# Kernel optimization log

Hardware: AMD Instinct MI355X
Metric: run time of the kernel (lower is better)

The kernel has to match this reference:

```python
import jax, jax.numpy as jnp
import numpy as np

N = 524288
L = 16            # encoding levels
F = 2             # features per level
LOG2_T = 19
T = 2 ** LOG2_T   # hash table size per level
BASE_RES = 16
FINEST = BASE_RES * 2 ** (L - 1)
WIDTH = 64
DENSITY_OUT = 16

# corner offsets of a voxel, i (x) outer, k (z) inner -- matches BOX_OFFSETS
OFFSETS = jnp.array([[i, j, k] for i in (0, 1) for j in (0, 1) for k in (0, 1)], dtype=jnp.int32)  # [8,3]
# primes wrapped to int32 exactly as jax x32 canonicalization does in the original
PRIMES = jnp.asarray(np.array([1, 2654435761, 805459861], dtype=np.int64).astype(np.int32))
_b = np.exp((np.log(FINEST) - np.log(BASE_RES)) / (L - 1))
RESOLUTIONS = jnp.asarray(np.floor(BASE_RES * _b ** np.arange(L)).astype(np.float32))  # [L]


def sh_encode(d):
    """Spherical harmonic encoding, degree 4 -> [N,25], faithful to source coeffs."""
    x, y, z = d[..., 0:1], d[..., 1:2], d[..., 2:3]
    x2, y2, z2 = x * x, y * y, z * z
    xy, xz, yz = x * y, x * z, y * z
    x4, y4 = x2 * x2, y2 * y2
    out = [jnp.full_like(x, 0.5 * np.sqrt(1.0 / np.pi))]
    c1 = 0.5 * np.sqrt(3.0 / np.pi)
    out += [-c1 * y, c1 * z, -c1 * x]
    sub = 0.25 * np.sqrt(5.0 / np.pi)
    v1 = 0.25 * np.sqrt(15.0 / np.pi)
    v2 = 0.5 * np.sqrt(15.0 / np.pi)
    v3 = 0.75 * np.sqrt(5.0 / np.pi)
    out += [v2 * xy, -v2 * yz, v3 * z2 - sub, -v2 * xz, v1 * x2 - v1 * y2]
    w1 = 0.25 * np.sqrt(105.0 / np.pi)
    w2 = 0.5 * np.sqrt(105.0 / np.pi)
    w3 = 0.25 * np.sqrt(35.0 / (2.0 * np.pi))
    w4 = 0.5 * np.sqrt(7.0 / (6.0 * np.pi))
    out += [-w3 * y * (3.0 * x2 - y2), w2 * xy * z, w4 * y * (1.5 - 7.5 * z2),
            1.24392110863372 * z * (1.5 * z2 - 0.5) - 0.497568443453487 * z,
            w4 * x * (1.5 - 7.5 * z2), w1 * z * (x2 - y2), -w3 * x * (x2 - 3.0 * y2)]
    out += [2.5033429417967 * xy * (x2 - y2),
            -1.77013076977993 * yz * (3.0 * x2 - y2),
            0.126156626101008 * xy * (52.5 * z2 - 7.5),
            0.267618617422916 * y * (2.33333333333333 * z * (1.5 - 7.5 * z2) + 4.0 * z),
            1.48099765681286 * z * (1.66666666666667 * z * (1.5 * z2 - 0.5) - 0.666666666666667 * z) - 0.952069922236839 * z2 + 0.317356640745613,
            0.267618617422916 * x * (2.33333333333333 * z * (1.5 - 7.5 * z2) + 4.0 * z),
            0.063078313050504 * (x2 - y2) * (52.5 * z2 - 7.5),
            -1.77013076977993 * xz * (x2 - 3.0 * y2),
            -3.75501441269506 * x2 * y2 + 0.625835735449176 * x4 + 0.625835735449176 * y4]
    return jnp.concatenate(out, axis=-1)  # [N,25]


def hash_grid_encode(x, tables):
    """x: [N,3] in unit cube; tables: [L,T,F] -> [N, L*F]."""
    def level(table, res):
        grid = 1.0 / res                              # box is [0,1]^3
        bl = jnp.floor(x / grid).astype(jnp.int32)    # bottom-left voxel index [N,3]
        w = (x - bl.astype(x.dtype) * grid) / grid    # trilinear weights [N,3]
        idx = bl[:, None, :] + OFFSETS[None]          # [N,8,3]
        h = ((idx[..., 0] * PRIMES[0]) ^ (idx[..., 1] * PRIMES[1]) ^ (idx[..., 2] * PRIMES[2])) % T
        emb = table[h]                                # [N,8,F] gather
        cw = jnp.where(OFFSETS[None].astype(bool), w[:, None, :], 1.0 - w[:, None, :]).prod(-1)  # [N,8]
        return jnp.einsum('ncf,nc->nf', emb, cw)
    feats = jax.vmap(level)(tables, RESOLUTIONS)      # [L,N,F]
    return jnp.transpose(feats, (1, 0, 2)).reshape(x.shape[0], L * F)


def setup_inputs() -> dict:
    key = jax.random.key(0)
    ks = jax.random.split(key, 8)
    position = jax.random.uniform(ks[0], (N, 3), jnp.float32)
    direction = jax.random.normal(ks[1], (N, 3), jnp.float32)
    hash_tables = jax.random.uniform(ks[2], (L, T, F), jnp.float32, -1e-4, 1e-4)
    def dense(k, fan_in, fan_out):
        return (jax.random.normal(k, (fan_in, fan_out), jnp.float32) / np.sqrt(fan_in),
                jnp.zeros((fan_out,), jnp.float32))
    W_d1, b_d1 = dense(ks[3], L * F, WIDTH)
    W_d2, b_d2 = dense(ks[4], WIDTH, DENSITY_OUT)
    W_c1, b_c1 = dense(ks[5], DENSITY_OUT + 25, WIDTH)
    W_c2, b_c2 = dense(ks[6], WIDTH, WIDTH)
    W_c3, b_c3 = dense(ks[7], WIDTH, 3)
    return dict(position=position, direction=direction, hash_tables=hash_tables,
                W_d1=W_d1, b_d1=b_d1, W_d2=W_d2, b_d2=b_d2,
                W_c1=W_c1, b_c1=b_c1, W_c2=W_c2, b_c2=b_c2, W_c3=W_c3, b_c3=b_c3)


def reference(position, direction, hash_tables, W_d1, b_d1, W_d2, b_d2,
              W_c1, b_c1, W_c2, b_c2, W_c3, b_c3):
    enc_pos = hash_grid_encode(position, hash_tables)     # [N,32]
    enc_dir = sh_encode(direction)                        # [N,25]
    y = jax.nn.relu(enc_pos @ W_d1 + b_d1)                # density MLP (1 hidden layer)
    density_out = y @ W_d2 + b_d2                         # [N,16]
    sigma = jax.nn.relu(density_out[:, -1:])              # [N,1]
    h = jnp.concatenate([density_out, enc_dir], axis=-1)  # [N,41]
    h = jax.nn.relu(h @ W_c1 + b_c1)
    h = jax.nn.relu(h @ W_c2 + b_c2)
    rgb = jax.nn.sigmoid(h @ W_c3 + b_c3)                 # [N,3]
    return (rgb, sigma)
```

## Files before the change

kernel.cpp:

```cpp
#include <hip/hip_runtime.h>
#include <math.h>

#define LEVELS 16
#define TBL 524288
#define TMASK (TBL - 1)

typedef short bf16x8 __attribute__((ext_vector_type(8)));
typedef float f32x4  __attribute__((ext_vector_type(4)));
typedef float fvec4  __attribute__((ext_vector_type(4)));
typedef unsigned int uvec4 __attribute__((ext_vector_type(4)));

static __device__ __forceinline__ unsigned short f2bf(float x) {
    unsigned u = __float_as_uint(x);
    u += 0x7fffu + ((u >> 16) & 1u);
    return (unsigned short)(u >> 16);
}
static __device__ __forceinline__ float b2f(unsigned short h) {
    return __uint_as_float(((unsigned)h) << 16);
}

#define SH_BLOCK(sh, dx, dy, dz)                                                          \
    const float x2 = dx * dx, y2 = dy * dy, z2 = dz * dz;                                 \
    const float xy = dx * dy, xz = dx * dz, yz = dy * dz;                                 \
    const float x4 = x2 * x2, y4 = y2 * y2;                                               \
    const float c0  = (float)(0.5 * sqrt(1.0 / M_PI));                                    \
    const float c1  = (float)(0.5 * sqrt(3.0 / M_PI));                                    \
    const float sub = (float)(0.25 * sqrt(5.0 / M_PI));                                   \
    const float v1  = (float)(0.25 * sqrt(15.0 / M_PI));                                  \
    const float v2  = (float)(0.5 * sqrt(15.0 / M_PI));                                   \
    const float v3  = (float)(0.75 * sqrt(5.0 / M_PI));                                   \
    const float w1c = (float)(0.25 * sqrt(105.0 / M_PI));                                 \
    const float w2c = (float)(0.5 * sqrt(105.0 / M_PI));                                  \
    const float w3c = (float)(0.25 * sqrt(35.0 / (2.0 * M_PI)));                          \
    const float w4c = (float)(0.5 * sqrt(7.0 / (6.0 * M_PI)));                            \
    sh[0] = c0;                                                                           \
    sh[1] = -c1 * dy;                                                                     \
    sh[2] =  c1 * dz;                                                                     \
    sh[3] = -c1 * dx;                                                                     \
    sh[4] =  v2 * xy;                                                                     \
    sh[5] = -v2 * yz;                                                                     \
    sh[6] =  v3 * z2 - sub;                                                               \
    sh[7] = -v2 * xz;                                                                     \
    sh[8] =  v1 * x2 - v1 * y2;                                                           \
    sh[9]  = -w3c * dy * (3.0f * x2 - y2);                                                \
    sh[10] =  w2c * xy * dz;                                                              \
    sh[11] =  w4c * dy * (1.5f - 7.5f * z2);                                              \
    sh[12] =  1.24392110863372f * dz * (1.5f * z2 - 0.5f) - 0.497568443453487f * dz;      \
    sh[13] =  w4c * dx * (1.5f - 7.5f * z2);                                              \
    sh[14] =  w1c * dz * (x2 - y2);                                                       \
    sh[15] = -w3c * dx * (x2 - 3.0f * y2);                                                \
    sh[16] =  2.5033429417967f * xy * (x2 - y2);                                          \
    sh[17] = -1.77013076977993f * yz * (3.0f * x2 - y2);                                  \
    sh[18] =  0.126156626101008f * xy * (52.5f * z2 - 7.5f);                              \
    sh[19] =  0.267618617422916f * dy * (2.33333333333333f * dz * (1.5f - 7.5f * z2) + 4.0f * dz); \
    sh[20] =  1.48099765681286f * dz * (1.66666666666667f * dz * (1.5f * z2 - 0.5f) - 0.666666666666667f * dz) \
              - 0.952069922236839f * z2 + 0.317356640745613f;                             \
    sh[21] =  0.267618617422916f * dx * (2.33333333333333f * dz * (1.5f - 7.5f * z2) + 4.0f * dz); \
    sh[22] =  0.063078313050504f * (x2 - y2) * (52.5f * z2 - 7.5f);                       \
    sh[23] = -1.77013076977993f * xz * (x2 - 3.0f * y2);                                  \
    sh[24] = -3.75501441269506f * x2 * y2 + 0.625835735449176f * x4 + 0.625835735449176f * y4;

__global__ __launch_bounds__(256)
void cvt_tables(const float* __restrict__ tables,
                unsigned int* __restrict__ tb16, int total)
{
    const int i = (blockIdx.x * 256 + threadIdx.x) * 4;
    if (i >= total) return;
    const fvec4 a = __builtin_nontemporal_load((const fvec4*)(tables + 2 * (size_t)i));
    const fvec4 b = __builtin_nontemporal_load((const fvec4*)(tables + 2 * (size_t)i) + 1);
    uvec4 o;
    o.x = ((unsigned)f2bf(a.y) << 16) | f2bf(a.x);
    o.y = ((unsigned)f2bf(a.w) << 16) | f2bf(a.z);
    o.z = ((unsigned)f2bf(b.y) << 16) | f2bf(b.x);
    o.w = ((unsigned)f2bf(b.w) << 16) | f2bf(b.z);
    __builtin_nontemporal_store(o, (uvec4*)&tb16[i]);
}

__global__ __launch_bounds__(256)
void ngp_encode_lvl(const float* __restrict__ pos,
                    const unsigned int* __restrict__ tb16,
                    unsigned int* __restrict__ wsp, int n)
{
    const int b = blockIdx.x;
    const int p = b & 7;
    const int h = b >> 14;
    const int l = 2 * p + h;
    const int c = (b & 16383) >> 3;
    const int idx = c * 256 + threadIdx.x;
    if (idx >= n || l >= LEVELS) return;

    const float px = pos[3 * idx + 0];
    const float py = pos[3 * idx + 1];
    const float pz = pos[3 * idx + 2];

    const float resf = (float)(16 << l);
    const float tx = px * resf, ty = py * resf, tz = pz * resf;
    const float fx = floorf(tx), fy = floorf(ty), fz = floorf(tz);
    const float wx = tx - fx, wy = ty - fy, wz = tz - fz;
    const unsigned ix = (unsigned)(int)fx;
    const unsigned iy = (unsigned)(int)fy;
    const unsigned iz = (unsigned)(int)fz;
    const unsigned hy0 = iy * 2654435761u, hy1 = hy0 + 2654435761u;
    const unsigned hz0 = iz * 805459861u,  hz1 = hz0 + 805459861u;
    const unsigned ix1 = ix + 1u;

    const unsigned int* tb = tb16 + (size_t)l * TBL;
    const unsigned hA = hy0 ^ hz0;
    const unsigned hB = hy0 ^ hz1;
    const unsigned hC = hy1 ^ hz0;
    const unsigned hD = hy1 ^ hz1;

    unsigned eA0, eA1, eB0, eB1, eC0, eC1, eD0, eD1;
    if ((ix & 1u) == 0u) {
        const uint2 pA = *(const uint2*)&tb[((ix ^ hA) & TMASK) & ~1u];
        const uint2 pB = *(const uint2*)&tb[((ix ^ hB) & TMASK) & ~1u];
        const uint2 pC = *(const uint2*)&tb[((ix ^ hC) & TMASK) & ~1u];
        const uint2 pD = *(const uint2*)&tb[((ix ^ hD) & TMASK) & ~1u];
        const unsigned sA = hA & 1u, sB = hB & 1u, sC = hC & 1u, sD = hD & 1u;
        eA0 = sA ? pA.y : pA.x;  eA1 = sA ? pA.x : pA.y;
        eB0 = sB ? pB.y : pB.x;  eB1 = sB ? pB.x : pB.y;
        eC0 = sC ? pC.y : pC.x;  eC1 = sC ? pC.x : pC.y;
        eD0 = sD ? pD.y : pD.x;  eD1 = sD ? pD.x : pD.y;
    } else {
        eA0 = tb[(ix  ^ hA) & TMASK];  eA1 = tb[(ix1 ^ hA) & TMASK];
        eB0 = tb[(ix  ^ hB) & TMASK];  eB1 = tb[(ix1 ^ hB) & TMASK];
        eC0 = tb[(ix  ^ hC) & TMASK];  eC1 = tb[(ix1 ^ hC) & TMASK];
        eD0 = tb[(ix  ^ hD) & TMASK];  eD1 = tb[(ix1 ^ hD) & TMASK];
    }

#define UNPX(e) __uint_as_float((e) << 16)
#define UNPY(e) __uint_as_float((e) & 0xffff0000u)

    const float ux = 1.f - wx, uy = 1.f - wy, uz = 1.f - wz;
    const float c000 = ux * uy * uz, c001 = ux * uy * wz;
    const float c010 = ux * wy * uz, c011 = ux * wy * wz;
    const float c100 = wx * uy * uz, c101 = wx * uy * wz;
    const float c110 = wx * wy * uz, c111 = wx * wy * wz;

    float f0 = UNPX(eA0) * c000, f1 = UNPY(eA0) * c000;
    f0 = fmaf(UNPX(eB0), c001, f0); f1 = fmaf(UNPY(eB0), c001, f1);
    f0 = fmaf(UNPX(eC0), c010, f0); f1 = fmaf(UNPY(eC0), c010, f1);
    f0 = fmaf(UNPX(eD0), c011, f0); f1 = fmaf(UNPY(eD0), c011, f1);
    f0 = fmaf(UNPX(eA1), c100, f0); f1 = fmaf(UNPY(eA1), c100, f1);
    f0 = fmaf(UNPX(eB1), c101, f0); f1 = fmaf(UNPY(eB1), c101, f1);
    f0 = fmaf(UNPX(eC1), c110, f0); f1 = fmaf(UNPY(eC1), c110, f1);
    f0 = fmaf(UNPX(eD1), c111, f0); f1 = fmaf(UNPY(eD1), c111, f1);

    const unsigned int h0 = f2bf(f0);
    const unsigned int h1 = f2bf(f1);
    __builtin_nontemporal_store((h1 << 16) | h0, &wsp[(size_t)l * n + idx]);
}

#define MT   512
#define GROUPS 8
#define SW1  32
#define SW   72
#define SA   68
#define OW1  0
#define OW2  2048
#define OC1H 3200
#define OC1L 7808
#define OC2H 12416
#define OC2L 17024
#define OC3H 21632
#define OC3L 21920
#define WTOT 22208

__global__ __launch_bounds__(512, 4)
void ngp_mlp_mfma4(const unsigned int* __restrict__ wsp,
                   const float* __restrict__ dirp,
                   const float* __restrict__ Wd1, const float* __restrict__ bd1,
                   const float* __restrict__ Wd2, const float* __restrict__ bd2,
                   const float* __restrict__ Wc1, const float* __restrict__ bc1,
                   const float* __restrict__ Wc2, const float* __restrict__ bc2,
                   const float* __restrict__ Wc3, const float* __restrict__ bc3,
                   float* __restrict__ out, int n)
{
    __shared__ short wsm[WTOT];
    __shared__ float act[8 * 16 * SA];
    const int tid = threadIdx.x;

    for (int t = tid; t < WTOT; t += MT) wsm[t] = 0;
    __syncthreads();

    for (int g = tid; g < 32 * 64; g += MT) {
        const int k = g >> 6, nn = g & 63;
        wsm[OW1 + nn * SW1 + k] = f2bf(Wd1[g]);
    }
    for (int g = tid; g < 64 * 16; g += MT) {
        const int k = g >> 4, nn = g & 15;
        wsm[OW2 + nn * SW + k] = f2bf(Wd2[g]);
    }
    for (int g = tid; g < 41 * 64; g += MT) {
        const int k = g >> 6, nn = g & 63;
        const float w = Wc1[g];
        const unsigned short hh = f2bf(w);
        wsm[OC1H + nn * SW + k] = hh;
        wsm[OC1L + nn * SW + k] = f2bf(w - b2f(hh));
    }
    for (int g = tid; g < 64 * 64; g += MT) {
        const int k = g >> 6, nn = g & 63;
        const float w = Wc2[g];
        const unsigned short hh = f2bf(w);
        wsm[OC2H + nn * SW + k] = hh;
        wsm[OC2L + nn * SW + k] = f2bf(w - b2f(hh));
    }
    for (int g = tid; g < 64 * 3; g += MT) {
        const int k = g / 3, nn = g - 3 * k;
        const float w = Wc3[g];
        const unsigned short hh = f2bf(w);
        wsm[OC3H + nn * SW + k] = hh;
        wsm[OC3L + nn * SW + k] = f2bf(w - b2f(hh));
    }
    __syncthreads();

    const int wid = tid >> 6;
    const int lane = tid & 63;
    const int ln = lane & 15;
    const int qd = lane >> 4;
    float* A = act + wid * (16 * SA);

    float bd1v[4], bc1v[4], bc2v[4];
#pragma unroll
    for (int t = 0; t < 4; ++t) {
        bd1v[t] = bd1[t * 16 + ln];
        bc1v[t] = bc1[t * 16 + ln];
        bc2v[t] = bc2[t * 16 + ln];
    }
    const float bd2v = bd2[ln];
    const float bc3v = (ln < 3) ? bc3[ln] : 0.f;

#define LOAD_SPLIT(ah, al, k0)                                   \
    {                                                            \
        _Pragma("unroll")                                        \
        for (int j = 0; j < 8; ++j) {                            \
            const float v = A[ln * SA + (k0) + j];               \
            const unsigned short hb = f2bf(v);                   \
            ah[j] = (short)hb;                                   \
            al[j] = (short)f2bf(v - b2f(hb));                    \
        }                                                        \
    }

#define SPLIT_TILE(acc, ah0, ah1, al0, al1, OH, OL, row)                                          \
    {                                                                                             \
        const bf16x8 bh0 = *(const bf16x8*)&wsm[(OH) + (row) * SW + qd * 8];                      \
        const bf16x8 bh1 = *(const bf16x8*)&wsm[(OH) + (row) * SW + 32 + qd * 8];                 \
        acc = __builtin_amdgcn_mfma_f32_16x16x32_bf16(ah0, bh0, acc, 0, 0, 0);                    \
        acc = __builtin_amdgcn_mfma_f32_16x16x32_bf16(ah1, bh1, acc, 0, 0, 0);                    \
        acc = __builtin_amdgcn_mfma_f32_16x16x32_bf16(al0, bh0, acc, 0, 0, 0);                    \
        acc = __builtin_amdgcn_mfma_f32_16x16x32_bf16(al1, bh1, acc, 0, 0, 0);                    \
        const bf16x8 bl0 = *(const bf16x8*)&wsm[(OL) + (row) * SW + qd * 8];                      \
        const bf16x8 bl1 = *(const bf16x8*)&wsm[(OL) + (row) * SW + 32 + qd * 8];                 \
        acc = __builtin_amdgcn_mfma_f32_16x16x32_bf16(ah0, bl0, acc, 0, 0, 0);                    \
        acc = __builtin_amdgcn_mfma_f32_16x16x32_bf16(ah1, bl1, acc, 0, 0, 0);                    \
    }

    const int pt0 = blockIdx.x * (GROUPS * 128) + wid * 16 + ln;
    unsigned int xu0, xu1, xu2, xu3;
    float dq0, dq1, dq2;
    xu0 = wsp[(size_t)(qd * 4 + 0) * n + pt0];
    xu1 = wsp[(size_t)(qd * 4 + 1) * n + pt0];
    xu2 = wsp[(size_t)(qd * 4 + 2) * n + pt0];
    xu3 = wsp[(size_t)(qd * 4 + 3) * n + pt0];
    dq0 = dirp[3 * pt0 + 0];
    dq1 = dirp[3 * pt0 + 1];
    dq2 = dirp[3 * pt0 + 2];

#pragma unroll 1
    for (int grp = 0; grp < GROUPS; ++grp) {
        const int pt_base = blockIdx.x * (GROUPS * 128) + grp * 128 + wid * 16;
        const int pt = pt_base + ln;

        bf16x8 ax;
        ax[0] = (short)(xu0 & 0xffffu); ax[1] = (short)(xu0 >> 16);
        ax[2] = (short)(xu1 & 0xffffu); ax[3] = (short)(xu1 >> 16);
        ax[4] = (short)(xu2 & 0xffffu); ax[5] = (short)(xu2 >> 16);
        ax[6] = (short)(xu3 & 0xffffu); ax[7] = (short)(xu3 >> 16);
        const float ddx = dq0, ddy = dq1, ddz = dq2;

        if (grp + 1 < GROUPS) {
            const int ptn = pt + 128;
            xu0 = wsp[(size_t)(qd * 4 + 0) * n + ptn];
            xu1 = wsp[(size_t)(qd * 4 + 1) * n + ptn];
            xu2 = wsp[(size_t)(qd * 4 + 2) * n + ptn];
            xu3 = wsp[(size_t)(qd * 4 + 3) * n + ptn];
            dq0 = dirp[3 * ptn + 0];
            dq1 = dirp[3 * ptn + 1];
            dq2 = dirp[3 * ptn + 2];
        }

#pragma unroll
        for (int t = 0; t < 4; ++t) {
            const bf16x8 b = *(const bf16x8*)&wsm[OW1 + (t * 16 + ln) * SW1 + qd * 8];
            const float bv = bd1v[t];
            f32x4 acc = {bv, bv, bv, bv};
            acc = __builtin_amdgcn_mfma_f32_16x16x32_bf16(ax, b, acc, 0, 0, 0);
#pragma unroll
            for (int r = 0; r < 4; ++r)
                A[(qd * 4 + r) * SA + t * 16 + ln] = fmaxf(acc[r], 0.f);
        }

        {
            bf16x8 a0, a1;
#pragma unroll
            for (int j = 0; j < 8; ++j) a0[j] = (short)f2bf(A[ln * SA + qd * 8 + j]);
#pragma unroll
            for (int j = 0; j < 8; ++j) a1[j] = (short)f2bf(A[ln * SA + 32 + qd * 8 + j]);
            const bf16x8 b0 = *(const bf16x8*)&wsm[OW2 + ln * SW + qd * 8];
            const bf16x8 b1 = *(const bf16x8*)&wsm[OW2 + ln * SW + 32 + qd * 8];
            const float bv = bd2v;
            f32x4 acc = {bv, bv, bv, bv};
            acc = __builtin_amdgcn_mfma_f32_16x16x32_bf16(a0, b0, acc, 0, 0, 0);
            acc = __builtin_amdgcn_mfma_f32_16x16x32_bf16(a1, b1, acc, 0, 0, 0);
            if (ln == 15) {
#pragma unroll
                for (int r = 0; r < 4; ++r)
                    out[3 * n + pt_base + qd * 4 + r] = fmaxf(acc[r], 0.f);
            }
#pragma unroll
            for (int r = 0; r < 4; ++r)
                A[(qd * 4 + r) * SA + ln] = acc[r];
        }

        {
            const float dxv = ddx, dyv = ddy, dzv = ddz;
            const float x2 = dxv * dxv, y2 = dyv * dyv, z2 = dzv * dzv;
            const float xy = dxv * dyv, xz = dxv * dzv, yz = dyv * dzv;
            const float x4 = x2 * x2, y4 = y2 * y2;
            const float c0  = (float)(0.5 * sqrt(1.0 / M_PI));
            const float c1  = (float)(0.5 * sqrt(3.0 / M_PI));
            const float sub = (float)(0.25 * sqrt(5.0 / M_PI));
            const float v1  = (float)(0.25 * sqrt(15.0 / M_PI));
            const float v2  = (float)(0.5 * sqrt(15.0 / M_PI));
            const float v3  = (float)(0.75 * sqrt(5.0 / M_PI));
            const float w1c = (float)(0.25 * sqrt(105.0 / M_PI));
            const float w2c = (float)(0.5 * sqrt(105.0 / M_PI));
            const float w3c = (float)(0.25 * sqrt(35.0 / (2.0 * M_PI)));
            const float w4c = (float)(0.5 * sqrt(7.0 / (6.0 * M_PI)));
            float* Ash = &A[ln * SA + 16];
#define SH_PUT(i, expr) { if (((i) & 3) == qd) Ash[i] = (expr); }
            SH_PUT(0,  c0)
            SH_PUT(1,  -c1 * dyv)
            SH_PUT(2,   c1 * dzv)
            SH_PUT(3,  -c1 * dxv)
            SH_PUT(4,   v2 * xy)
            SH_PUT(5,  -v2 * yz)
            SH_PUT(6,   v3 * z2 - sub)
            SH_PUT(7,  -v2 * xz)
            SH_PUT(8,   v1 * x2 - v1 * y2)
            SH_PUT(9,  -w3c * dyv * (3.0f * x2 - y2))
            SH_PUT(10,  w2c * xy * dzv)
            SH_PUT(11,  w4c * dyv * (1.5f - 7.5f * z2))
            SH_PUT(12,  1.24392110863372f * dzv * (1.5f * z2 - 0.5f) - 0.497568443453487f * dzv)
            SH_PUT(13,  w4c * dxv * (1.5f - 7.5f * z2))
            SH_PUT(14,  w1c * dzv * (x2 - y2))
            SH_PUT(15, -w3c * dxv * (x2 - 3.0f * y2))
            SH_PUT(16,  2.5033429417967f * xy * (x2 - y2))
            SH_PUT(17, -1.77013076977993f * yz * (3.0f * x2 - y2))
            SH_PUT(18,  0.126156626101008f * xy * (52.5f * z2 - 7.5f))
            SH_PUT(19,  0.267618617422916f * dyv * (2.33333333333333f * dzv * (1.5f - 7.5f * z2) + 4.0f * dzv))
            SH_PUT(20,  1.48099765681286f * dzv * (1.66666666666667f * dzv * (1.5f * z2 - 0.5f) - 0.666666666666667f * dzv)
                        - 0.952069922236839f * z2 + 0.317356640745613f)
            SH_PUT(21,  0.267618617422916f * dxv * (2.33333333333333f * dzv * (1.5f - 7.5f * z2) + 4.0f * dzv))
            SH_PUT(22,  0.063078313050504f * (x2 - y2) * (52.5f * z2 - 7.5f))
            SH_PUT(23, -1.77013076977993f * xz * (x2 - 3.0f * y2))
            SH_PUT(24, -3.75501441269506f * x2 * y2 + 0.625835735449176f * x4 + 0.625835735449176f * y4)
#undef SH_PUT
        }

        {
            bf16x8 ah0, ah1, al0, al1;
            LOAD_SPLIT(ah0, al0, qd * 8)
            LOAD_SPLIT(ah1, al1, 32 + qd * 8)
#pragma unroll
            for (int t = 0; t < 4; ++t) {
                const float bv = bc1v[t];
                f32x4 acc = {bv, bv, bv, bv};
                SPLIT_TILE(acc, ah0, ah1, al0, al1, OC1H, OC1L, t * 16 + ln)
#pragma unroll
                for (int r = 0; r < 4; ++r)
                    A[(qd * 4 + r) * SA + t * 16 + ln] = fmaxf(acc[r], 0.f);
                __builtin_amdgcn_sched_barrier(0);
            }
        }

        {
            bf16x8 ah0, ah1, al0, al1;
            LOAD_SPLIT(ah0, al0, qd * 8)
            LOAD_SPLIT(ah1, al1, 32 + qd * 8)
#pragma unroll
            for (int t = 0; t < 4; ++t) {
                const float bv = bc2v[t];
                f32x4 acc = {bv, bv, bv, bv};
                SPLIT_TILE(acc, ah0, ah1, al0, al1, OC2H, OC2L, t * 16 + ln)
#pragma unroll
                for (int r = 0; r < 4; ++r)
                    A[(qd * 4 + r) * SA + t * 16 + ln] = fmaxf(acc[r], 0.f);
                __builtin_amdgcn_sched_barrier(0);
            }
        }

        {
            bf16x8 ah0, ah1, al0, al1;
            LOAD_SPLIT(ah0, al0, qd * 8)
            LOAD_SPLIT(ah1, al1, 32 + qd * 8)
            const float bv = bc3v;
            f32x4 acc = {bv, bv, bv, bv};
            SPLIT_TILE(acc, ah0, ah1, al0, al1, OC3H, OC3L, (ln & 3))
            if (ln < 3) {
#pragma unroll
                for (int r = 0; r < 4; ++r)
                    out[3 * (pt_base + qd * 4 + r) + ln] = 1.f / (1.f + expf(-acc[r]));
            }
        }
    }
}

__global__ __launch_bounds__(256)
void nerf_fused(const float* __restrict__ pos,
                const float* __restrict__ dirp,
                const float* __restrict__ tables,
                const float* __restrict__ Wd1, const float* __restrict__ bd1,
                const float* __restrict__ Wd2, const float* __restrict__ bd2,
                const float* __restrict__ Wc1, const float* __restrict__ bc1,
                const float* __restrict__ Wc2, const float* __restrict__ bc2,
                const float* __restrict__ Wc3, const float* __restrict__ bc3,
                float* __restrict__ out, int n)
{
    const int idx = blockIdx.x * blockDim.x + threadIdx.x;
    if (idx >= n) return;
    const float px = pos[3 * idx + 0], py = pos[3 * idx + 1], pz = pos[3 * idx + 2];
    float y[64];
#pragma unroll
    for (int j = 0; j < 64; ++j) y[j] = bd1[j];
#pragma unroll
    for (int l = 0; l < LEVELS; ++l) {
        const float resf = (float)(16 << l);
        const float tx = px * resf, ty = py * resf, tz = pz * resf;
        const float fx = floorf(tx), fy = floorf(ty), fz = floorf(tz);
        const float wx = tx - fx, wy = ty - fy, wz = tz - fz;
        const unsigned ix = (unsigned)(int)fx, iy = (unsigned)(int)fy, iz = (unsigned)(int)fz;
        const unsigned hy0 = iy * 2654435761u, hy1 = hy0 + 2654435761u;
        const unsigned hz0 = iz * 805459861u,  hz1 = hz0 + 805459861u;
        const unsigned ix1 = ix + 1u;
        const float2* tb = (const float2*)tables + (size_t)l * TBL;
        const float2 e000 = tb[(ix  ^ hy0 ^ hz0) & TMASK];
        const float2 e001 = tb[(ix  ^ hy0 ^ hz1) & TMASK];
        const float2 e010 = tb[(ix  ^ hy1 ^ hz0) & TMASK];
        const float2 e011 = tb[(ix  ^ hy1 ^ hz1) & TMASK];
        const float2 e100 = tb[(ix1 ^ hy0 ^ hz0) & TMASK];
        const float2 e101 = tb[(ix1 ^ hy0 ^ hz1) & TMASK];
        const float2 e110 = tb[(ix1 ^ hy1 ^ hz0) & TMASK];
        const float2 e111 = tb[(ix1 ^ hy1 ^ hz1) & TMASK];
        const float ux = 1.f - wx, uy = 1.f - wy, uz = 1.f - wz;
        const float c000 = ux*uy*uz, c001 = ux*uy*wz, c010 = ux*wy*uz, c011 = ux*wy*wz;
        const float c100 = wx*uy*uz, c101 = wx*uy*wz, c110 = wx*wy*uz, c111 = wx*wy*wz;
        float f0 = e000.x*c000, f1 = e000.y*c000;
        f0 = fmaf(e001.x,c001,f0); f1 = fmaf(e001.y,c001,f1);
        f0 = fmaf(e010.x,c010,f0); f1 = fmaf(e010.y,c010,f1);
        f0 = fmaf(e011.x,c011,f0); f1 = fmaf(e011.y,c011,f1);
        f0 = fmaf(e100.x,c100,f0); f1 = fmaf(e100.y,c100,f1);
        f0 = fmaf(e101.x,c101,f0); f1 = fmaf(e101.y,c101,f1);
        f0 = fmaf(e110.x,c110,f0); f1 = fmaf(e110.y,c110,f1);
        f0 = fmaf(e111.x,c111,f0); f1 = fmaf(e111.y,c111,f1);
        const float* w0 = Wd1 + (size_t)(2 * l) * 64;
#pragma unroll
        for (int j = 0; j < 64; ++j)
            y[j] = fmaf(f0, w0[j], fmaf(f1, w0[64 + j], y[j]));
    }
    float d[16];
#pragma unroll
    for (int k = 0; k < 16; ++k) d[k] = bd2[k];
#pragma unroll
    for (int j = 0; j < 64; ++j) {
        const float a = fmaxf(y[j], 0.f);
#pragma unroll
        for (int k = 0; k < 16; ++k) d[k] = fmaf(a, Wd2[j * 16 + k], d[k]);
    }
    out[3 * n + idx] = fmaxf(d[15], 0.f);
    const float dx = dirp[3*idx], dy = dirp[3*idx+1], dz = dirp[3*idx+2];
    float sh[25];
    SH_BLOCK(sh, dx, dy, dz)
    float h1[64];
#pragma unroll
    for (int j = 0; j < 64; ++j) h1[j] = bc1[j];
#pragma unroll
    for (int i = 0; i < 16; ++i) {
#pragma unroll
        for (int j = 0; j < 64; ++j) h1[j] = fmaf(d[i], Wc1[i * 64 + j], h1[j]);
    }
#pragma unroll
    for (int s = 0; s < 25; ++s) {
#pragma unroll
        for (int j = 0; j < 64; ++j) h1[j] = fmaf(sh[s], Wc1[(16 + s) * 64 + j], h1[j]);
    }
    float h2[64];
#pragma unroll
    for (int j = 0; j < 64; ++j) h2[j] = bc2[j];
#pragma unroll
    for (int i = 0; i < 64; ++i) {
        const float a = fmaxf(h1[i], 0.f);
#pragma unroll
        for (int j = 0; j < 64; ++j) h2[j] = fmaf(a, Wc2[i * 64 + j], h2[j]);
    }
    float r0 = bc3[0], r1 = bc3[1], r2 = bc3[2];
#pragma unroll
    for (int j = 0; j < 64; ++j) {
        const float a = fmaxf(h2[j], 0.f);
        r0 = fmaf(a, Wc3[j * 3 + 0], r0);
        r1 = fmaf(a, Wc3[j * 3 + 1], r1);
        r2 = fmaf(a, Wc3[j * 3 + 2], r2);
    }
    out[3 * idx + 0] = 1.f / (1.f + expf(-r0));
    out[3 * idx + 1] = 1.f / (1.f + expf(-r1));
    out[3 * idx + 2] = 1.f / (1.f + expf(-r2));
}

extern "C" void kernel_launch(void* const* d_in, const int* in_sizes, int n_in,
                              void* d_out, int out_size, void* d_ws, size_t ws_size,
                              hipStream_t stream) {
    const float* pos    = (const float*)d_in[0];
    const float* dir    = (const float*)d_in[1];
    const float* tables = (const float*)d_in[2];
    const float* Wd1 = (const float*)d_in[3];
    const float* bd1 = (const float*)d_in[4];
    const float* Wd2 = (const float*)d_in[5];
    const float* bd2 = (const float*)d_in[6];
    const float* Wc1 = (const float*)d_in[7];
    const float* bc1 = (const float*)d_in[8];
    const float* Wc2 = (const float*)d_in[9];
    const float* bc2 = (const float*)d_in[10];
    const float* Wc3 = (const float*)d_in[11];
    const float* bc3 = (const float*)d_in[12];

    const int n = in_sizes[0] / 3;
    const int blocks = (n + 255) / 256;

    if (ws_size >= (size_t)n * 128 && n == 524288) {
        unsigned int* wsp  = (unsigned int*)d_ws;
        unsigned int* tb16 = (unsigned int*)((char*)d_ws + (size_t)n * 64);
        const int total = LEVELS * TBL;
        cvt_tables<<<total / 1024, 256, 0, stream>>>(tables, tb16, total);
        ngp_encode_lvl<<<16 * blocks, 256, 0, stream>>>(pos, tb16, wsp, n);
        ngp_mlp_mfma4<<<n / (128 * GROUPS), MT, 0, stream>>>((const unsigned int*)wsp, dir,
                                                             Wd1, bd1, Wd2, bd2,
                                                             Wc1, bc1, Wc2, bc2, Wc3, bc3,
                                                             (float*)d_out, n);
    } else {
        nerf_fused<<<blocks, 256, 0, stream>>>(pos, dir, tables,
                                               Wd1, bd1, Wd2, bd2,
                                               Wc1, bc1, Wc2, bc2, Wc3, bc3,
                                               (float*)d_out, n);
    }
}
```

Before: 355.3 us.

## Fuse hash-grid encoding into MLP kernel via shared-memory feature staging

```diff
diff --git a/kernel.cpp b/kernel.cpp
--- a/kernel.cpp
+++ b/kernel.cpp
@@ -76,83 +76,7 @@
     __builtin_nontemporal_store(o, (uvec4*)&tb16[i]);
 }
 
-__global__ __launch_bounds__(256)
-void ngp_encode_lvl(const float* __restrict__ pos,
-                    const unsigned int* __restrict__ tb16,
-                    unsigned int* __restrict__ wsp, int n)
-{
-    const int b = blockIdx.x;
-    const int p = b & 7;
-    const int h = b >> 14;
-    const int l = 2 * p + h;
-    const int c = (b & 16383) >> 3;
-    const int idx = c * 256 + threadIdx.x;
-    if (idx >= n || l >= LEVELS) return;
-
-    const float px = pos[3 * idx + 0];
-    const float py = pos[3 * idx + 1];
-    const float pz = pos[3 * idx + 2];
-
-    const float resf = (float)(16 << l);
-    const float tx = px * resf, ty = py * resf, tz = pz * resf;
-    const float fx = floorf(tx), fy = floorf(ty), fz = floorf(tz);
-    const float wx = tx - fx, wy = ty - fy, wz = tz - fz;
-    const unsigned ix = (unsigned)(int)fx;
-    const unsigned iy = (unsigned)(int)fy;
-    const unsigned iz = (unsigned)(int)fz;
-    const unsigned hy0 = iy * 2654435761u, hy1 = hy0 + 2654435761u;
-    const unsigned hz0 = iz * 805459861u,  hz1 = hz0 + 805459861u;
-    const unsigned ix1 = ix + 1u;
-
-    const unsigned int* tb = tb16 + (size_t)l * TBL;
-    const unsigned hA = hy0 ^ hz0;
-    const unsigned hB = hy0 ^ hz1;
-    const unsigned hC = hy1 ^ hz0;
-    const unsigned hD = hy1 ^ hz1;
-
-    unsigned eA0, eA1, eB0, eB1, eC0, eC1, eD0, eD1;
-    if ((ix & 1u) == 0u) {
-        const uint2 pA = *(const uint2*)&tb[((ix ^ hA) & TMASK) & ~1u];
-        const uint2 pB = *(const uint2*)&tb[((ix ^ hB) & TMASK) & ~1u];
-        const uint2 pC = *(const uint2*)&tb[((ix ^ hC) & TMASK) & ~1u];
-        const uint2 pD = *(const uint2*)&tb[((ix ^ hD) & TMASK) & ~1u];
-        const unsigned sA = hA & 1u, sB = hB & 1u, sC = hC & 1u, sD = hD & 1u;
-        eA0 = sA ? pA.y : pA.x;  eA1 = sA ? pA.x : pA.y;
-        eB0 = sB ? pB.y : pB.x;  eB1 = sB ? pB.x : pB.y;
-        eC0 = sC ? pC.y : pC.x;  eC1 = sC ? pC.x : pC.y;
-        eD0 = sD ? pD.y : pD.x;  eD1 = sD ? pD.x : pD.y;
-    } else {
-        eA0 = tb[(ix  ^ hA) & TMASK];  eA1 = tb[(ix1 ^ hA) & TMASK];
-        eB0 = tb[(ix  ^ hB) & TMASK];  eB1 = tb[(ix1 ^ hB) & TMASK];
-        eC0 = tb[(ix  ^ hC) & TMASK];  eC1 = tb[(ix1 ^ hC) & TMASK];
-        eD0 = tb[(ix  ^ hD) & TMASK];  eD1 = tb[(ix1 ^ hD) & TMASK];
-    }
-
-#define UNPX(e) __uint_as_float((e) << 16)
-#define UNPY(e) __uint_as_float((e) & 0xffff0000u)
-
-    const float ux = 1.f - wx, uy = 1.f - wy, uz = 1.f - wz;
-    const float c000 = ux * uy * uz, c001 = ux * uy * wz;
-    const float c010 = ux * wy * uz, c011 = ux * wy * wz;
-    const float c100 = wx * uy * uz, c101 = wx * uy * wz;
-    const float c110 = wx * wy * uz, c111 = wx * wy * wz;
-
-    float f0 = UNPX(eA0) * c000, f1 = UNPY(eA0) * c000;
-    f0 = fmaf(UNPX(eB0), c001, f0); f1 = fmaf(UNPY(eB0), c001, f1);
-    f0 = fmaf(UNPX(eC0), c010, f0); f1 = fmaf(UNPY(eC0), c010, f1);
-    f0 = fmaf(UNPX(eD0), c011, f0); f1 = fmaf(UNPY(eD0), c011, f1);
-    f0 = fmaf(UNPX(eA1), c100, f0); f1 = fmaf(UNPY(eA1), c100, f1);
-    f0 = fmaf(UNPX(eB1), c101, f0); f1 = fmaf(UNPY(eB1), c101, f1);
-    f0 = fmaf(UNPX(eC1), c110, f0); f1 = fmaf(UNPY(eC1), c110, f1);
-    f0 = fmaf(UNPX(eD1), c111, f0); f1 = fmaf(UNPY(eD1), c111, f1);
-
-    const unsigned int h0 = f2bf(f0);
-    const unsigned int h1 = f2bf(f1);
-    __builtin_nontemporal_store((h1 << 16) | h0, &wsp[(size_t)l * n + idx]);
-}
-
-#define MT   512
-#define GROUPS 8
+#define GROUPS_F 4
 #define SW1  32
 #define SW   72
 #define SA   68
@@ -166,51 +90,116 @@
 #define OC3L 21920
 #define WTOT 22208
 
-__global__ __launch_bounds__(512, 4)
-void ngp_mlp_mfma4(const unsigned int* __restrict__ wsp,
-                   const float* __restrict__ dirp,
-                   const float* __restrict__ Wd1, const float* __restrict__ bd1,
-                   const float* __restrict__ Wd2, const float* __restrict__ bd2,
-                   const float* __restrict__ Wc1, const float* __restrict__ bc1,
-                   const float* __restrict__ Wc2, const float* __restrict__ bc2,
-                   const float* __restrict__ Wc3, const float* __restrict__ bc3,
-                   float* __restrict__ out, int n)
+__global__ __launch_bounds__(256, 2)
+void ngp_fused(const float* __restrict__ pos,
+               const unsigned int* __restrict__ tb16,
+               const float* __restrict__ dirp,
+               const float* __restrict__ Wd1, const float* __restrict__ bd1,
+               const float* __restrict__ Wd2, const float* __restrict__ bd2,
+               const float* __restrict__ Wc1, const float* __restrict__ bc1,
+               const float* __restrict__ Wc2, const float* __restrict__ bc2,
+               const float* __restrict__ Wc3, const float* __restrict__ bc3,
+               float* __restrict__ out, int n)
 {
     __shared__ short wsm[WTOT];
-    __shared__ float act[8 * 16 * SA];
+    __shared__ unsigned int xf[256 * 16];
+    __shared__ float act[4 * 16 * SA];
     const int tid = threadIdx.x;
 
-    for (int t = tid; t < WTOT; t += MT) wsm[t] = 0;
+    for (int t = tid; t < WTOT; t += 256) wsm[t] = 0;
     __syncthreads();
-
-    for (int g = tid; g < 32 * 64; g += MT) {
+    for (int g = tid; g < 32 * 64; g += 256) {
         const int k = g >> 6, nn = g & 63;
         wsm[OW1 + nn * SW1 + k] = f2bf(Wd1[g]);
     }
-    for (int g = tid; g < 64 * 16; g += MT) {
+    for (int g = tid; g < 64 * 16; g += 256) {
         const int k = g >> 4, nn = g & 15;
         wsm[OW2 + nn * SW + k] = f2bf(Wd2[g]);
     }
-    for (int g = tid; g < 41 * 64; g += MT) {
+    for (int g = tid; g < 41 * 64; g += 256) {
         const int k = g >> 6, nn = g & 63;
         const float w = Wc1[g];
         const unsigned short hh = f2bf(w);
         wsm[OC1H + nn * SW + k] = hh;
         wsm[OC1L + nn * SW + k] = f2bf(w - b2f(hh));
     }
-    for (int g = tid; g < 64 * 64; g += MT) {
+    for (int g = tid; g < 64 * 64; g += 256) {
         const int k = g >> 6, nn = g & 63;
         const float w = Wc2[g];
         const unsigned short hh = f2bf(w);
         wsm[OC2H + nn * SW + k] = hh;
         wsm[OC2L + nn * SW + k] = f2bf(w - b2f(hh));
     }
-    for (int g = tid; g < 64 * 3; g += MT) {
+    for (int g = tid; g < 64 * 3; g += 256) {
         const int k = g / 3, nn = g - 3 * k;
         const float w = Wc3[g];
         const unsigned short hh = f2bf(w);
         wsm[OC3H + nn * SW + k] = hh;
         wsm[OC3L + nn * SW + k] = f2bf(w - b2f(hh));
+    }
+
+    {
+        const int ptg = blockIdx.x * 256 + tid;
+        const float px = pos[3 * ptg + 0];
+        const float py = pos[3 * ptg + 1];
+        const float pz = pos[3 * ptg + 2];
+#pragma unroll 2
+        for (int l = 0; l < LEVELS; ++l) {
+            const float resf = (float)(16 << l);
+            const float tx = px * resf, ty = py * resf, tz = pz * resf;
+            const float fx = floorf(tx), fy = floorf(ty), fz = floorf(tz);
+            const float wx = tx - fx, wy = ty - fy, wz = tz - fz;
+            const unsigned ix = (unsigned)(int)fx;
+            const unsigned iy = (unsigned)(int)fy;
+            const unsigned iz = (unsigned)(int)fz;
+            const unsigned hy0 = iy * 2654435761u, hy1 = hy0 + 2654435761u;
+            const unsigned hz0 = iz * 805459861u,  hz1 = hz0 + 805459861u;
+            const unsigned ix1 = ix + 1u;
+
+            const unsigned int* tb = tb16 + (size_t)l * TBL;
+            const unsigned hA = hy0 ^ hz0;
+            const unsigned hB = hy0 ^ hz1;
+            const unsigned hC = hy1 ^ hz0;
+            const unsigned hD = hy1 ^ hz1;
+
+            unsigned eA0, eA1, eB0, eB1, eC0, eC1, eD0, eD1;
+            if ((ix & 1u) == 0u) {
+                const uint2 pA = *(const uint2*)&tb[((ix ^ hA) & TMASK) & ~1u];
+                const uint2 pB = *(const uint2*)&tb[((ix ^ hB) & TMASK) & ~1u];
+                const uint2 pC = *(const uint2*)&tb[((ix ^ hC) & TMASK) & ~1u];
+                const uint2 pD = *(const uint2*)&tb[((ix ^ hD) & TMASK) & ~1u];
+                const unsigned sA = hA & 1u, sB = hB & 1u, sC = hC & 1u, sD = hD & 1u;
+                eA0 = sA ? pA.y : pA.x;  eA1 = sA ? pA.x : pA.y;
+                eB0 = sB ? pB.y : pB.x;  eB1 = sB ? pB.x : pB.y;
+                eC0 = sC ? pC.y : pC.x;  eC1 = sC ? pC.x : pC.y;
+                eD0 = sD ? pD.y : pD.x;  eD1 = sD ? pD.x : pD.y;
+            } else {
+                eA0 = tb[(ix  ^ hA) & TMASK];  eA1 = tb[(ix1 ^ hA) & TMASK];
+                eB0 = tb[(ix  ^ hB) & TMASK];  eB1 = tb[(ix1 ^ hB) & TMASK];
+                eC0 = tb[(ix  ^ hC) & TMASK];  eC1 = tb[(ix1 ^ hC) & TMASK];
+                eD0 = tb[(ix  ^ hD) & TMASK];  eD1 = tb[(ix1 ^ hD) & TMASK];
+            }
+
+#define UNPX(e) __uint_as_float((e) << 16)
+#define UNPY(e) __uint_as_float((e) & 0xffff0000u)
+
+            const float ux = 1.f - wx, uy = 1.f - wy, uz = 1.f - wz;
+            const float c000 = ux * uy * uz, c001 = ux * uy * wz;
+            const float c010 = ux * wy * uz, c011 = ux * wy * wz;
+            const float c100 = wx * uy * uz, c101 = wx * uy * wz;
+            const float c110 = wx * wy * uz, c111 = wx * wy * wz;
+
+            float f0 = UNPX(eA0) * c000, f1 = UNPY(eA0) * c000;
+            f0 = fmaf(UNPX(eB0), c001, f0); f1 = fmaf(UNPY(eB0), c001, f1);
+            f0 = fmaf(UNPX(eC0), c010, f0); f1 = fmaf(UNPY(eC0), c010, f1);
+            f0 = fmaf(UNPX(eD0), c011, f0); f1 = fmaf(UNPY(eD0), c011, f1);
+            f0 = fmaf(UNPX(eA1), c100, f0); f1 = fmaf(UNPY(eA1), c100, f1);
+            f0 = fmaf(UNPX(eB1), c101, f0); f1 = fmaf(UNPY(eB1), c101, f1);
+            f0 = fmaf(UNPX(eC1), c110, f0); f1 = fmaf(UNPY(eC1), c110, f1);
+            f0 = fmaf(UNPX(eD1), c111, f0); f1 = fmaf(UNPY(eD1), c111, f1);
+
+            xf[tid * 16 + l] = ((unsigned)f2bf(f1) << 16) | f2bf(f0);
+        }
     }
     __syncthreads();
 
@@ -255,35 +244,29 @@
         acc = __builtin_amdgcn_mfma_f32_16x16x32_bf16(ah1, bl1, acc, 0, 0, 0);                    \
     }
 
-    const int pt0 = blockIdx.x * (GROUPS * 128) + wid * 16 + ln;
-    unsigned int xu0, xu1, xu2, xu3;
-    float dq0, dq1, dq2;
-    xu0 = wsp[(size_t)(qd * 4 + 0) * n + pt0];
-    xu1 = wsp[(size_t)(qd * 4 + 1) * n + pt0];
-    xu2 = wsp[(size_t)(qd * 4 + 2) * n + pt0];
-    xu3 = wsp[(size_t)(qd * 4 + 3) * n + pt0];
-    dq0 = dirp[3 * pt0 + 0];
-    dq1 = dirp[3 * pt0 + 1];
-    dq2 = dirp[3 * pt0 + 2];
+    const int pt0 = blockIdx.x * 256 + wid * 64 + ln;
+    float dq0 = dirp[3 * pt0 + 0];
+    float dq1 = dirp[3 * pt0 + 1];
+    float dq2 = dirp[3 * pt0 + 2];
 
 #pragma unroll 1
-    for (int grp = 0; grp < GROUPS; ++grp) {
-        const int pt_base = blockIdx.x * (GROUPS * 128) + grp * 128 + wid * 16;
+    for (int grp = 0; grp < GROUPS_F; ++grp) {
+        const int ptl_base = wid * 64 + grp * 16;
+        const int pt_base = blockIdx.x * 256 + ptl_base;
         const int pt = pt_base + ln;
 
         bf16x8 ax;
-        ax[0] = (short)(xu0 & 0xffffu); ax[1] = (short)(xu0 >> 16);
-        ax[2] = (short)(xu1 & 0xffffu); ax[3] = (short)(xu1 >> 16);
-        ax[4] = (short)(xu2 & 0xffffu); ax[5] = (short)(xu2 >> 16);
-        ax[6] = (short)(xu3 & 0xffffu); ax[7] = (short)(xu3 >> 16);
+        {
+            const uvec4 xr = *(const uvec4*)&xf[(ptl_base + ln) * 16 + qd * 4];
+            ax[0] = (short)(xr.x & 0xffffu); ax[1] = (short)(xr.x >> 16);
+            ax[2] = (short)(xr.y & 0xffffu); ax[3] = (short)(xr.y >> 16);
+            ax[4] = (short)(xr.z & 0xffffu); ax[5] = (short)(xr.z >> 16);
+            ax[6] = (short)(xr.w & 0xffffu); ax[7] = (short)(xr.w >> 16);
+        }
         const float ddx = dq0, ddy = dq1, ddz = dq2;
 
-        if (grp + 1 < GROUPS) {
-            const int ptn = pt + 128;
-            xu0 = wsp[(size_t)(qd * 4 + 0) * n + ptn];
-            xu1 = wsp[(size_t)(qd * 4 + 1) * n + ptn];
-            xu2 = wsp[(size_t)(qd * 4 + 2) * n + ptn];
-            xu3 = wsp[(size_t)(qd * 4 + 3) * n + ptn];
+        if (grp + 1 < GROUPS_F) {
+            const int ptn = pt + 16;
             dq0 = dirp[3 * ptn + 0];
             dq1 = dirp[3 * ptn + 1];
             dq2 = dirp[3 * ptn + 2];
@@ -536,16 +519,14 @@
     const int n = in_sizes[0] / 3;
     const int blocks = (n + 255) / 256;
 
-    if (ws_size >= (size_t)n * 128 && n == 524288) {
-        unsigned int* wsp  = (unsigned int*)d_ws;
-        unsigned int* tb16 = (unsigned int*)((char*)d_ws + (size_t)n * 64);
+    if (ws_size >= (size_t)LEVELS * TBL * 4 && n == 524288) {
+        unsigned int* tb16 = (unsigned int*)d_ws;
         const int total = LEVELS * TBL;
         cvt_tables<<<total / 1024, 256, 0, stream>>>(tables, tb16, total);
-        ngp_encode_lvl<<<16 * blocks, 256, 0, stream>>>(pos, tb16, wsp, n);
-        ngp_mlp_mfma4<<<n / (128 * GROUPS), MT, 0, stream>>>((const unsigned int*)wsp, dir,
-                                                             Wd1, bd1, Wd2, bd2,
-                                                             Wc1, bc1, Wc2, bc2, Wc3, bc3,
-                                                             (float*)d_out, n);
+        ngp_fused<<<n / 256, 256, 0, stream>>>(pos, tb16, dir,
+                                               Wd1, bd1, Wd2, bd2,
+                                               Wc1, bc1, Wc2, bc2, Wc3, bc3,
+                                               (float*)d_out, n);
     } else {
         nerf_fused<<<blocks, 256, 0, stream>>>(pos, dir, tables,
                                                Wd1, bd1, Wd2, bd2,
```

New measurement: 430.1 us. +21.1%, slower.
